# Performance work log

Measured on AMD Instinct MI355X. Metric: run time of the kernel, lower is better.

The kernel has to match this reference:

```python
import jax, jax.numpy as jnp
import numpy as np

GATE_SLOPE = 10.0
ALPHA = 0.8
KH = KW = 3
PAD = 1
STRIDE = 1


def setup_inputs() -> dict:
    key = jax.random.key(0)
    ks = jax.random.split(key, 7)
    B, Cin, H, W = 4, 16, 32, 32
    Cout, NB = 32, 3
    pshape = (Cout, Cin, NB, KH, KW)
    x = jax.random.normal(ks[0], (B, Cin, H, W), dtype=jnp.float32)
    k = jax.random.uniform(ks[1], pshape, dtype=jnp.float32) * 2.0 + 0.5
    Ec = jax.random.uniform(ks[2], pshape, dtype=jnp.float32) * 2.0 + 0.5
    Ps = jax.random.uniform(ks[3], pshape, dtype=jnp.float32) * 1.5 + 0.5
    bias = jax.random.normal(ks[4], pshape, dtype=jnp.float32) * 0.1
    coef = jax.random.normal(ks[5], pshape, dtype=jnp.float32)
    out_bias = jnp.zeros((Cout,), dtype=jnp.float32)
    return {"x": x, "k": k, "Ec": Ec, "Ps": Ps, "bias": bias, "coef": coef, "out_bias": out_bias}


def _unfold(x):
    # x: (B, Cin, H, W) -> (B, Cin, kH, kW, L) like F.unfold with pad/stride
    B, Cin, H, W = x.shape
    Hout = (H + 2 * PAD - KH) // STRIDE + 1
    Wout = (W + 2 * PAD - KW) // STRIDE + 1
    xp = jnp.pad(x, ((0, 0), (0, 0), (PAD, PAD), (PAD, PAD)))
    patches = jnp.stack(
        [xp[:, :, i:i + Hout * STRIDE:STRIDE, j:j + Wout * STRIDE:STRIDE]
         for i in range(KH) for j in range(KW)], axis=2)  # (B,Cin,kH*kW,Hout,Wout)
    return patches.reshape(B, Cin, KH, KW, Hout * Wout), Hout, Wout


def reference(x, k, Ec, Ps, bias, coef, out_bias):
    B, Cin, H, W = x.shape
    Cout = k.shape[0]
    x_exp, Hout, Wout = _unfold(x)  # (B,Cin,kH,kW,L)
    # stateful=False: prev_x = stop_gradient(x), branch = 1.0
    dx = x_exp - jax.lax.stop_gradient(x_exp)
    is_up = jax.nn.sigmoid(GATE_SLOPE * dx)  # value 0.5, nonzero grad path
    # broadcast axes: x -> (B,1,Cin,1,kH,kW,L); params -> (1,Cout,Cin,NB,kH,kW,1)
    x7 = x_exp[:, None, :, None]
    up7 = is_up[:, None, :, None]
    kc, Ecc, Psc, bc, cc = (p[None, ..., None] for p in (k, Ec, Ps, bias, coef))
    crossed_pos = jax.nn.sigmoid(GATE_SLOPE * (x7 - Ecc))
    crossed_neg = jax.nn.sigmoid(GATE_SLOPE * (-x7 - Ecc))
    sw_up = up7 * crossed_pos
    sw_lo = (1.0 - up7) * crossed_neg
    branch = 1.0
    target_sign = sw_up - sw_lo + (1.0 - sw_up - sw_lo) * branch
    branch_momentum = ALPHA * branch + (1.0 - ALPHA) * target_sign
    shifted = x7 + Ecc * branch_momentum
    basis = Psc * jnp.tanh(kc * shifted) + bc
    out = jnp.sum(basis * cc, axis=(2, 3, 4, 5))  # (B,Cout,L)
    out = out.reshape(B, Cout, Hout, Wout) + out_bias[None, :, None, None]
    return out
```

## Files before the change

kernel.cpp:

```cpp
#include <hip/hip_runtime.h>

#define LOG2E 1.4426950408889634f
#define C1 (10.0f * LOG2E)

__global__ __launch_bounds__(256, 6) void fused_kernel(
    const float* __restrict__ x, const float* __restrict__ kk,
    const float* __restrict__ Ec, const float* __restrict__ Ps,
    const float* __restrict__ bias, const float* __restrict__ coef,
    const float* __restrict__ out_bias, float* __restrict__ out) {
    __shared__ float2 sX[2176];
    __shared__ float4 sP[432];
    __shared__ float  red[256];
    __shared__ float  wK0[4];

    const int bid = blockIdx.x, tid = threadIdx.x;
    const int chunk = bid & 15;
    const int co    = (bid >> 4) & 31;
    const int b     = bid >> 9;

    for (int t = tid; t < 2176; t += 256) {
        int ci  = t / 136;
        int rem = t - ci * 136;
        int r   = rem / 34;
        int c   = rem - r * 34;
        int row = chunk * 2 + r - 1;
        int col = c - 1;
        float xv = 0.f;
        if ((unsigned)row < 32u && (unsigned)col < 32u)
            xv = x[((b * 16 + ci) << 10) + (row << 5) + col];
        sX[t] = make_float2(xv, __builtin_amdgcn_exp2f(C1 * xv));
    }

    float kpart = 0.f;
    for (int t = tid; t < 432; t += 256) {
        int ci = t / 27;
        int r2 = t - ci * 27;
        int j  = r2 / 3;
        int nb = r2 - j * 3;
        int i  = co * 432 + ci * 27 + nb * 9 + j;
        float e  = Ec[i];
        float zk = 2.0f * LOG2E * kk[i];
        float ps = Ps[i], cf = coef[i];
        sP[t] = make_float4(__builtin_amdgcn_exp2f(C1 * e), zk, zk * e, 2.0f * ps * cf);
        kpart += cf * (ps + bias[i]);
    }
    #pragma unroll
    for (int off = 32; off >= 1; off >>= 1) kpart += __shfl_down(kpart, off, 64);
    if ((tid & 63) == 0) wK0[tid >> 6] = kpart;
    __syncthreads();

    const int px = tid & 63;
    const int w  = px & 31;
    const int hr = px >> 5;
    const int cb = (tid >> 6) << 2;

    float a0 = 0.f, a1 = 0.f, a2 = 0.f;
    #pragma unroll
    for (int i = 0; i < 4; ++i) {
        const float2* xw = &sX[(cb + i) * 136 + hr * 34 + w];
        float2 X[9];
        #pragma unroll
        for (int j = 0; j < 9; ++j)
            X[j] = xw[(j / 3) * 34 + (j % 3)];
        const float4* pc = &sP[(cb + i) * 27];
        #pragma unroll
        for (int j = 0; j < 9; ++j) {
            const float xv = X[j].x, E1 = X[j].y;
            const float4 P0 = pc[j * 3 + 0];
            const float4 P1 = pc[j * 3 + 1];
            const float4 P2 = pc[j * 3 + 2];
            float cn0 = __builtin_amdgcn_rcpf(__builtin_fmaf(E1, P0.x, 1.f));
            float cn1 = __builtin_amdgcn_rcpf(__builtin_fmaf(E1, P1.x, 1.f));
            float cn2 = __builtin_amdgcn_rcpf(__builtin_fmaf(E1, P2.x, 1.f));
            float t0 = __builtin_fmaf(P0.y, xv, P0.z);
            float t1 = __builtin_fmaf(P1.y, xv, P1.z);
            float t2 = __builtin_fmaf(P2.y, xv, P2.z);
            float u0 = __builtin_fmaf(-0.2f * P0.z, cn0, t0);
            float u1 = __builtin_fmaf(-0.2f * P1.z, cn1, t1);
            float u2 = __builtin_fmaf(-0.2f * P2.z, cn2, t2);
            float e0 = __builtin_amdgcn_exp2f(u0);
            float e1 = __builtin_amdgcn_exp2f(u1);
            float e2 = __builtin_amdgcn_exp2f(u2);
            float r0 = __builtin_amdgcn_rcpf(1.f + e0);
            float r1 = __builtin_amdgcn_rcpf(1.f + e1);
            float r2 = __builtin_amdgcn_rcpf(1.f + e2);
            a0 = __builtin_fmaf(-P0.w, r0, a0);
            a1 = __builtin_fmaf(-P1.w, r1, a1);
            a2 = __builtin_fmaf(-P2.w, r2, a2);
        }
    }
    red[tid] = a0 + a1 + a2;
    __syncthreads();
    if (tid < 64) {
        float r = red[tid] + red[tid + 64] + red[tid + 128] + red[tid + 192];
        float k0 = wK0[0] + wK0[1] + wK0[2] + wK0[3] + out_bias[co];
        int o = ((b * 32 + co) << 10) + (chunk << 6) + tid;
        out[o] = r + k0;
    }
}

extern "C" void kernel_launch(void* const* d_in, const int* in_sizes, int n_in,
                              void* d_out, int out_size, void* d_ws, size_t ws_size,
                              hipStream_t stream) {
    const float* x        = (const float*)d_in[0];
    const float* k        = (const float*)d_in[1];
    const float* Ec       = (const float*)d_in[2];
    const float* Ps       = (const float*)d_in[3];
    const float* bias     = (const float*)d_in[4];
    const float* coef     = (const float*)d_in[5];
    const float* out_bias = (const float*)d_in[6];
    float* out = (float*)d_out;

    fused_kernel<<<2048, 256, 0, stream>>>(x, k, Ec, Ps, bias, coef, out_bias, out);
}
```

Measured before the change: 28.57 us.

## Shrink shared memory, precompute gate term, and raise occupancy bound

```diff
diff --git a/kernel.cpp b/kernel.cpp
--- a/kernel.cpp
+++ b/kernel.cpp
@@ -3,14 +3,14 @@
 #define LOG2E 1.4426950408889634f
 #define C1 (10.0f * LOG2E)
 
-__global__ __launch_bounds__(256, 6) void fused_kernel(
+__global__ __launch_bounds__(256, 8) void fused_kernel(
     const float* __restrict__ x, const float* __restrict__ kk,
     const float* __restrict__ Ec, const float* __restrict__ Ps,
     const float* __restrict__ bias, const float* __restrict__ coef,
     const float* __restrict__ out_bias, float* __restrict__ out) {
-    __shared__ float2 sX[2176];
+    __shared__ float  sX[2176];
     __shared__ float4 sP[432];
-    __shared__ float  red[256];
+    __shared__ float  sW[432];
     __shared__ float  wK0[4];
 
     const int bid = blockIdx.x, tid = threadIdx.x;
@@ -28,7 +28,7 @@
         float xv = 0.f;
         if ((unsigned)row < 32u && (unsigned)col < 32u)
             xv = x[((b * 16 + ci) << 10) + (row << 5) + col];
-        sX[t] = make_float2(xv, __builtin_amdgcn_exp2f(C1 * xv));
+        sX[t] = xv;
     }
 
     float kpart = 0.f;
@@ -40,8 +40,10 @@
         int i  = co * 432 + ci * 27 + nb * 9 + j;
         float e  = Ec[i];
         float zk = 2.0f * LOG2E * kk[i];
+        float a  = zk * e;
         float ps = Ps[i], cf = coef[i];
-        sP[t] = make_float4(__builtin_amdgcn_exp2f(C1 * e), zk, zk * e, 2.0f * ps * cf);
+        sP[t] = make_float4(__builtin_amdgcn_exp2f(C1 * e), zk, a, 0.2f * a);
+        sW[t] = 2.0f * ps * cf;
         kpart += cf * (ps + bias[i]);
     }
     #pragma unroll
@@ -57,38 +59,48 @@
     float a0 = 0.f, a1 = 0.f, a2 = 0.f;
     #pragma unroll
     for (int i = 0; i < 4; ++i) {
-        const float2* xw = &sX[(cb + i) * 136 + hr * 34 + w];
-        float2 X[9];
+        const float* xw = &sX[(cb + i) * 136 + hr * 34 + w];
+        float X[9], E[9];
         #pragma unroll
         for (int j = 0; j < 9; ++j)
             X[j] = xw[(j / 3) * 34 + (j % 3)];
+        #pragma unroll
+        for (int j = 0; j < 9; ++j)
+            E[j] = __builtin_amdgcn_exp2f(C1 * X[j]);
         const float4* pc = &sP[(cb + i) * 27];
+        const float*  wc = &sW[(cb + i) * 27];
         #pragma unroll
         for (int j = 0; j < 9; ++j) {
-            const float xv = X[j].x, E1 = X[j].y;
+            const float xv = X[j], E1 = E[j];
             const float4 P0 = pc[j * 3 + 0];
             const float4 P1 = pc[j * 3 + 1];
             const float4 P2 = pc[j * 3 + 2];
+            const float w0 = wc[j * 3 + 0];
+            const float w1 = wc[j * 3 + 1];
+            const float w2v = wc[j * 3 + 2];
             float cn0 = __builtin_amdgcn_rcpf(__builtin_fmaf(E1, P0.x, 1.f));
             float cn1 = __builtin_amdgcn_rcpf(__builtin_fmaf(E1, P1.x, 1.f));
             float cn2 = __builtin_amdgcn_rcpf(__builtin_fmaf(E1, P2.x, 1.f));
             float t0 = __builtin_fmaf(P0.y, xv, P0.z);
             float t1 = __builtin_fmaf(P1.y, xv, P1.z);
             float t2 = __builtin_fmaf(P2.y, xv, P2.z);
-            float u0 = __builtin_fmaf(-0.2f * P0.z, cn0, t0);
-            float u1 = __builtin_fmaf(-0.2f * P1.z, cn1, t1);
-            float u2 = __builtin_fmaf(-0.2f * P2.z, cn2, t2);
+            float u0 = __builtin_fmaf(-P0.w, cn0, t0);
+            float u1 = __builtin_fmaf(-P1.w, cn1, t1);
+            float u2 = __builtin_fmaf(-P2.w, cn2, t2);
             float e0 = __builtin_amdgcn_exp2f(u0);
             float e1 = __builtin_amdgcn_exp2f(u1);
             float e2 = __builtin_amdgcn_exp2f(u2);
             float r0 = __builtin_amdgcn_rcpf(1.f + e0);
             float r1 = __builtin_amdgcn_rcpf(1.f + e1);
             float r2 = __builtin_amdgcn_rcpf(1.f + e2);
-            a0 = __builtin_fmaf(-P0.w, r0, a0);
-            a1 = __builtin_fmaf(-P1.w, r1, a1);
-            a2 = __builtin_fmaf(-P2.w, r2, a2);
+            a0 = __builtin_fmaf(-w0, r0, a0);
+            a1 = __builtin_fmaf(-w1, r1, a1);
+            a2 = __builtin_fmaf(-w2v, r2, a2);
         }
     }
+
+    __syncthreads();
+    float* red = sX;
     red[tid] = a0 + a1 + a2;
     __syncthreads();
     if (tid < 64) {
```

Measured after the change: 27.81 us. -2.7%, faster.
